# Performance work log

Measured on AMD Instinct MI355X. Metric: run time of the kernel, lower is better.

Reference implementation:

```python
import jax, jax.numpy as jnp
import numpy as np

B, DIM, N_SIDE = 32, 256, 32
HEADS, DIM_K, DIM_U = 4, 16, 1
DIM_V = 64  # dim_out // heads
EPS = 1e-5

def _rel_pos_idx(n):
    # matches calc_rel_pos: meshgrid(ij) -> (N,2), pairwise diff + (n-1)
    i = np.arange(n)
    pos = np.stack(np.meshgrid(i, i, indexing='ij'), 0).reshape(2, -1).T  # (N, 2)
    rel = pos[None, :] - pos[:, None] + (n - 1)                            # (N, N, 2)
    return rel[..., 0], rel[..., 1]

def _bn(t, gamma, beta):
    # BatchNorm2d in training mode: batch stats over (B, H, W), biased var
    mu = t.mean(axis=(0, 2, 3), keepdims=True)
    var = t.var(axis=(0, 2, 3), keepdims=True)
    xhat = (t - mu) * jax.lax.rsqrt(var + EPS)
    return xhat * gamma[None, :, None, None] + beta[None, :, None, None]

def setup_inputs() -> dict:
    key = jax.random.key(0)
    ks = jax.random.split(key, 5)
    rl = 2 * N_SIDE - 1
    return {
        'x': jax.random.normal(ks[0], (B, DIM, N_SIDE, N_SIDE), jnp.float32),
        'w_q': jax.random.normal(ks[1], (DIM_K * HEADS, DIM), jnp.float32) * 0.05,
        'w_k': jax.random.normal(ks[2], (DIM_K * DIM_U, DIM), jnp.float32) * 0.05,
        'w_v': jax.random.normal(ks[3], (DIM_V * DIM_U, DIM), jnp.float32) * 0.05,
        'gamma_q': jnp.ones((DIM_K * HEADS,), jnp.float32),
        'beta_q': jnp.zeros((DIM_K * HEADS,), jnp.float32),
        'gamma_v': jnp.ones((DIM_V * DIM_U,), jnp.float32),
        'beta_v': jnp.zeros((DIM_V * DIM_U,), jnp.float32),
        'rel_pos_emb': jax.random.normal(ks[4], (rl, rl, DIM_K, DIM_U), jnp.float32),
    }

def reference(x, w_q, w_k, w_v, gamma_q, beta_q, gamma_v, beta_v, rel_pos_emb):
    b, c, hh, ww = x.shape
    n = hh * ww
    # 1x1 convs as channel contractions
    q = _bn(jnp.einsum('oc,bchw->bohw', w_q, x), gamma_q, beta_q)
    k = jnp.einsum('oc,bchw->bohw', w_k, x)
    v = _bn(jnp.einsum('oc,bchw->bohw', w_v, x), gamma_v, beta_v)
    q = q.reshape(b, HEADS, DIM_K, n)   # b h k n
    k = k.reshape(b, DIM_U, DIM_K, n)   # b u k m
    v = v.reshape(b, DIM_U, DIM_V, n)   # b u v m
    k = jax.nn.softmax(k, axis=-1)
    # content lambda
    lam_c = jnp.einsum('bukm,buvm->bkv', k, v)
    Yc = jnp.einsum('bhkn,bkv->bhvn', q, lam_c)
    # positional lambda via relative-position embedding gather
    ni, mi = _rel_pos_idx(N_SIDE)
    emb = rel_pos_emb[ni, mi]                      # (n, n, k, u)
    lam_p = jnp.einsum('nmku,buvm->bnkv', emb, v)  # dominant compute
    Yp = jnp.einsum('bhkn,bnkv->bhvn', q, lam_p)
    Y = Yc + Yp                                    # b h v n
    return Y.reshape(b, HEADS * DIM_V, hh, ww)
```

## Files before the change

### kernel.cpp

```cpp
#include <hip/hip_runtime.h>

using u16 = unsigned short;
using u32 = unsigned int;

typedef __attribute__((ext_vector_type(4))) float f32x4;
typedef __attribute__((ext_vector_type(4))) u16 u16x4;
typedef __attribute__((ext_vector_type(8))) u16 u16x8;
typedef __attribute__((ext_vector_type(8))) short s16x8;

__device__ __forceinline__ u16 f2bf(float f) {
  u32 x = __builtin_bit_cast(u32, f);
  x += 0x7fffu + ((x >> 16) & 1u);
  return (u16)(x >> 16);
}
__device__ __forceinline__ float bf2f(u16 u) {
  u32 x = ((u32)u) << 16;
  return __builtin_bit_cast(float, x);
}

__device__ __forceinline__ void glds16(const u16* gsrc, u16* ldst) {
  __builtin_amdgcn_global_load_lds(
      (const __attribute__((address_space(1))) unsigned int*)gsrc,
      (__attribute__((address_space(3))) unsigned int*)ldst, 16, 0, 0);
}

__global__ __launch_bounds__(256) void k_prep(
    const float* __restrict__ wq, const float* __restrict__ wk,
    const float* __restrict__ wv, const float* __restrict__ R,
    u16* __restrict__ Wb, u16* __restrict__ APre)
{
  const int blk = blockIdx.x;
  const int t = threadIdx.x;
  if (blk < 144) {
    const int o = blk;
    const float* src = (o < 64) ? (wq + o * 256)
                     : (o < 80) ? (wk + (o - 64) * 256)
                                : (wv + (o - 80) * 256);
    Wb[o * 256 + t] = f2bf(src[t]);
  } else {
    const int di = blk - 144;
    const int w = t >> 6, l = t & 63;
    const int g = l >> 4, k = l & 15;
    for (int j1 = w; j1 < 32; j1 += 4) {
      u16x8 o8;
#pragma unroll
      for (int e = 0; e < 8; ++e) {
        int dj = 8 * g + e - j1 + 31;
        o8[e] = f2bf(R[(di * 63 + dj) * 16 + k]);
      }
      *(u16x8*)(APre + ((di * 32 + j1) * 64 + l) * 8) = o8;
    }
  }
}

union ProjSmem {
  u16 XLb[64][264];
  float SS[2][160];
};

__global__ __launch_bounds__(256) void k_proj(
    const float* __restrict__ x, const u16* __restrict__ Wb,
    float* __restrict__ q_raw, float* __restrict__ k_raw,
    float* __restrict__ v_raw,
    float* __restrict__ qs1, float* __restrict__ qs2,
    float* __restrict__ vs1, float* __restrict__ vs2)
{
  __shared__ ProjSmem PS;
  const int b  = blockIdx.x >> 4;
  const int p0 = (blockIdx.x & 15) * 64;
  const int t  = threadIdx.x;

  {
    const int p4 = (t & 15) * 4;
    const int cb = (t >> 4);
#pragma unroll
    for (int i = 0; i < 8; ++i) {
      const int c = 2 * (i * 16 + cb);
      f32x4 xa = *(const f32x4*)&x[(b * 256 + c) * 1024 + p0 + p4];
      f32x4 xb = *(const f32x4*)&x[(b * 256 + c + 1) * 1024 + p0 + p4];
#pragma unroll
      for (int j = 0; j < 4; ++j) {
        u32 pk = (u32)f2bf(xa[j]) | ((u32)f2bf(xb[j]) << 16);
        *(u32*)&PS.XLb[p4 + j][c] = pk;
      }
    }
  }
  __syncthreads();

  const int w  = t >> 6;
  const int l  = t & 63;
  const int g  = l >> 4;
  const int cc = l & 15;
  const int p  = p0 + w * 16 + cc;

  f32x4 acc[9];
  const f32x4 fz = {0.f, 0.f, 0.f, 0.f};
#pragma unroll
  for (int mt = 0; mt < 9; ++mt) acc[mt] = fz;

#pragma unroll
  for (int ko = 0; ko < 8; ++ko) {
    s16x8 bfr = *(const s16x8*)&PS.XLb[w * 16 + cc][ko * 32 + g * 8];
#pragma unroll
    for (int mt = 0; mt < 9; ++mt) {
      s16x8 afr = *(const s16x8*)&Wb[(mt * 16 + cc) * 256 + ko * 32 + g * 8];
      acc[mt] = __builtin_amdgcn_mfma_f32_16x16x32_bf16(afr, bfr, acc[mt], 0, 0, 0);
    }
  }

#pragma unroll
  for (int mt = 0; mt < 9; ++mt) {
#pragma unroll
    for (int r = 0; r < 4; ++r) {
      const int o = mt * 16 + 4 * g + r;
      const float val = acc[mt][r];
      if (mt < 4)       q_raw[(b * 64 + o) * 1024 + p] = val;
      else if (mt == 4) k_raw[(b * 16 + (o - 64)) * 1024 + p] = val;
      else              v_raw[(b * 64 + (o - 80)) * 1024 + p] = val;
    }
  }

  __syncthreads();
  {
    float* ss = &PS.SS[0][0];
    for (int i = t; i < 320; i += 256) ss[i] = 0.f;
  }
  __syncthreads();
#pragma unroll
  for (int mt = 0; mt < 9; ++mt) {
    if (mt == 4) continue;
#pragma unroll
    for (int r = 0; r < 4; ++r) {
      float s1 = acc[mt][r];
      float s2 = s1 * s1;
#pragma unroll
      for (int off = 1; off < 16; off <<= 1) {
        s1 += __shfl_xor(s1, off);
        s2 += __shfl_xor(s2, off);
      }
      if (cc == 0) {
        const int o = mt * 16 + 4 * g + r;
        atomicAdd(&PS.SS[0][o], s1);
        atomicAdd(&PS.SS[1][o], s2);
      }
    }
  }
  __syncthreads();
  if (t < 64) {
    atomicAdd(&qs1[t], PS.SS[0][t]);
    atomicAdd(&qs2[t], PS.SS[1][t]);
  } else if (t >= 80 && t < 144) {
    atomicAdd(&vs1[t - 80], PS.SS[0][t]);
    atomicAdd(&vs2[t - 80], PS.SS[1][t]);
  }
}

__global__ __launch_bounds__(256) void k_soft(
    const float* __restrict__ k_raw,
    float* __restrict__ kmax, float* __restrict__ kinv)
{
  const int t = threadIdx.x;
  const int w = t >> 6, lane = t & 63;
  const int row = blockIdx.x * 4 + w;
  const f32x4* kr4 = (const f32x4*)(k_raw + row * 1024 + lane * 16);
  f32x4 a0 = kr4[0], a1 = kr4[1], a2 = kr4[2], a3 = kr4[3];
  float mx = -3.0e38f;
#pragma unroll
  for (int j = 0; j < 4; ++j)
    mx = fmaxf(mx, fmaxf(fmaxf(a0[j], a1[j]), fmaxf(a2[j], a3[j])));
#pragma unroll
  for (int off = 32; off; off >>= 1) mx = fmaxf(mx, __shfl_xor(mx, off));
  float s = 0.f;
#pragma unroll
  for (int j = 0; j < 4; ++j)
    s += __expf(a0[j] - mx) + __expf(a1[j] - mx)
       + __expf(a2[j] - mx) + __expf(a3[j] - mx);
#pragma unroll
  for (int off = 32; off; off >>= 1) s += __shfl_xor(s, off);
  if (lane == 0) { kmax[row] = mx; kinv[row] = 1.0f / s; }
}

__global__ __launch_bounds__(256) void k_nl(
    const float* __restrict__ v_raw,
    const float* __restrict__ vs1, const float* __restrict__ vs2,
    const float* __restrict__ gv, const float* __restrict__ bv,
    const float* __restrict__ k_raw, const float* __restrict__ kmax,
    const float* __restrict__ kinv,
    u16* __restrict__ vnF, float* __restrict__ lam_c)
{
  __shared__ float VN[64][136];
  __shared__ float KE[16][132];
  const int b  = blockIdx.x >> 3;
  const int m0 = (blockIdx.x & 7) * 128;
  const int t  = threadIdx.x;
  {
    const int v = t & 63, mseg = t >> 6;
    const float invN = 1.0f / 32768.0f;
    const float mu = vs1[v] * invN;
    const float var = vs2[v] * invN - mu * mu;
    const float sc = rsqrtf(var + 1e-5f) * gv[v];
    const float bi = bv[v] - mu * sc;
    const int i2 = (m0 >> 5) + mseg;
    const float* src = v_raw + (b * 64 + v) * 1024 + i2 * 32;
    u16* dstF = vnF + ((b * 32 + i2) * 4 + (v >> 4)) * 512 + (v & 15) * 8;
#pragma unroll
    for (int lg = 0; lg < 4; ++lg) {
      f32x4 a = *(const f32x4*)(src + lg * 8);
      f32x4 c = *(const f32x4*)(src + lg * 8 + 4);
      f32x4 na, nc;
      u16x8 o8;
#pragma unroll
      for (int j = 0; j < 4; ++j) {
        na[j] = a[j] * sc + bi;
        nc[j] = c[j] * sc + bi;
        o8[j] = f2bf(na[j]);
        o8[4 + j] = f2bf(nc[j]);
      }
      *(f32x4*)&VN[v][mseg * 32 + lg * 8] = na;
      *(f32x4*)&VN[v][mseg * 32 + lg * 8 + 4] = nc;
      *(u16x8*)(dstF + lg * 128) = o8;
    }
  }
  {
    const int kc = t >> 4, mm = (t & 15) * 8;
    const int row = b * 16 + kc;
    const float* kr = k_raw + row * 1024 + m0 + mm;
    const float mx = kmax[row], iv = kinv[row];
#pragma unroll
    for (int j = 0; j < 8; ++j) KE[kc][mm + j] = __expf(kr[j] - mx) * iv;
  }
  __syncthreads();
  const int kc = t & 15, vg = t >> 4;
  float acc[4] = {0.f, 0.f, 0.f, 0.f};
  for (int m4 = 0; m4 < 128; m4 += 4) {
    f32x4 ke = *(const f32x4*)&KE[kc][m4];
#pragma unroll
    for (int j = 0; j < 4; ++j) {
      f32x4 vv = *(const f32x4*)&VN[vg * 4 + j][m4];
      acc[j] += ke[0] * vv[0] + ke[1] * vv[1] + ke[2] * vv[2] + ke[3] * vv[3];
    }
  }
#pragma unroll
  for (int j = 0; j < 4; ++j)
    atomicAdd(&lam_c[(b * 16 + kc) * 64 + vg * 4 + j], acc[j]);
}

__device__ __forceinline__ void load_a4(s16x8 (&dst)[4], const u16* ab)
{
#pragma unroll
  for (int j = 0; j < 4; ++j) dst[j] = *(const s16x8*)(ab + j * 512);
}

union KMainSmem {
  u16 BB[2][8192];
  float YL[256][18];
};

__global__ __launch_bounds__(256, 4) void k_main(
    const u16* __restrict__ APre, const u16* __restrict__ vnF,
    const float* __restrict__ q_raw, const float* __restrict__ lam_c,
    const float* __restrict__ qs1, const float* __restrict__ qs2,
    const float* __restrict__ gq, const float* __restrict__ bq,
    float* __restrict__ out)
{
  __shared__ alignas(16) KMainSmem S;
  __shared__ float QL[64][17];
  const int bid  = blockIdx.x;
  const int xcd  = bid & 7;
  const int sb   = bid >> 3;
  const int b    = xcd * 4 + (sb & 3);
  const int rest = sb >> 2;
  const int i1   = rest >> 1;
  const int half = rest & 1;
  const int t  = threadIdx.x;
  const int w  = t >> 6;
  const int l  = t & 63;
  const int g  = l >> 4;
  const int c  = l & 15;
  const int j1base = half * 16 + w * 4;

  const u16* vF = vnF + b * 65536;

  f32x4 acc[4][4];
  const f32x4 fz = {0.f, 0.f, 0.f, 0.f};
#pragma unroll
  for (int nn = 0; nn < 4; ++nn)
#pragma unroll
    for (int tt = 0; tt < 4; ++tt) acc[nn][tt] = fz;

  {
    const int o = t >> 2, ns = (t & 3) * 4;
    const float invN = 1.0f / 32768.0f;
    const float mu = qs1[o] * invN;
    const float var = qs2[o] * invN - mu * mu;
    const float rs = rsqrtf(var + 1e-5f);
    const float sc = rs * gq[o];
    const float bi = bq[o] - mu * sc;
    f32x4 qa = *(const f32x4*)&q_raw[(b * 64 + o) * 1024 + i1 * 32 + half * 16 + ns];
#pragma unroll
    for (int j = 0; j < 4; ++j) QL[o][ns + j] = qa[j] * sc + bi;
  }
  {
    const u16* src = vF + w * 2048 + l * 8;
    u16* dst = &S.BB[0][w * 2048];
#pragma unroll
    for (int j = 0; j < 4; ++j) glds16(src + j * 512, dst + j * 512);
  }

  s16x8 afrP[4], afrQ[4];
  const u16* aBase = APre + ((31 - i1) * 32 + j1base) * 512 + l * 8;
  load_a4(afrP, aBase);
  __syncthreads();

  for (int p = 0; p < 8; ++p) {
    const int cur = p & 1;
    const bool pf = (p < 7);
    if (pf) {
      const u16* src = vF + (p + 1) * 8192 + w * 2048 + l * 8;
      u16* dst = &S.BB[cur ^ 1][w * 2048];
#pragma unroll
      for (int j = 0; j < 4; ++j) glds16(src + j * 512, dst + j * 512);
    }
    __builtin_amdgcn_sched_barrier(0);
    const u16* ap = aBase + 4 * p * 16384;
    s16x8 bfr[4];
#pragma unroll
    for (int s = 0; s < 4; ++s) {
#pragma unroll
      for (int tt = 0; tt < 4; ++tt)
        bfr[tt] = *(const s16x8*)&S.BB[cur][s * 2048 + tt * 512 + l * 8];
      if (s < 3) {
        if (s & 1) load_a4(afrP, ap + (s + 1) * 16384);
        else       load_a4(afrQ, ap + (s + 1) * 16384);
      } else if (pf) {
        load_a4(afrP, ap + 4 * 16384);
      }
      const s16x8* A = (s & 1) ? afrQ : afrP;
#pragma unroll
      for (int nn = 0; nn < 4; ++nn)
#pragma unroll
        for (int tt = 0; tt < 4; ++tt)
          acc[nn][tt] = __builtin_amdgcn_mfma_f32_16x16x32_bf16(
              A[nn], bfr[tt], acc[nn][tt], 0, 0, 0);
    }
    asm volatile("s_waitcnt vmcnt(4)" ::: "memory");
    __builtin_amdgcn_sched_barrier(0);
    __builtin_amdgcn_s_barrier();
    __builtin_amdgcn_sched_barrier(0);
  }

  {
    const float* lcb = lam_c + b * 1024;
#pragma unroll
    for (int tt = 0; tt < 4; ++tt)
#pragma unroll
      for (int r = 0; r < 4; ++r) {
        const float lv = lcb[(4 * g + r) * 64 + tt * 16 + c];
#pragma unroll
        for (int nn = 0; nn < 4; ++nn) acc[nn][tt][r] += lv;
      }
  }
#pragma unroll
  for (int nn = 0; nn < 4; ++nn) {
    const int j1loc = w * 4 + nn;
#pragma unroll
    for (int h = 0; h < 4; ++h) {
      const float q0 = QL[h * 16 + 4 * g + 0][j1loc];
      const float q1 = QL[h * 16 + 4 * g + 1][j1loc];
      const float q2 = QL[h * 16 + 4 * g + 2][j1loc];
      const float q3 = QL[h * 16 + 4 * g + 3][j1loc];
#pragma unroll
      for (int tt = 0; tt < 4; ++tt) {
        float sY = q0 * acc[nn][tt][0] + q1 * acc[nn][tt][1]
                 + q2 * acc[nn][tt][2] + q3 * acc[nn][tt][3];
        sY += __shfl_xor(sY, 16);
        sY += __shfl_xor(sY, 32);
        if (g == h) S.YL[h * 64 + tt * 16 + c][j1loc] = sY;
      }
    }
  }
  __syncthreads();
#pragma unroll
  for (int it = 0; it < 4; ++it) {
    const int o  = (t >> 2) + it * 64;
    const int nf = (t & 3) * 4;
    f32x4 v4 = *(const f32x4*)&S.YL[o][nf];
    *(f32x4*)&out[(b * 256 + o) * 1024 + i1 * 32 + half * 16 + nf] = v4;
  }
}

extern "C" void kernel_launch(void* const* d_in, const int* in_sizes, int n_in,
                              void* d_out, int out_size, void* d_ws, size_t ws_size,
                              hipStream_t stream) {
  const float* x  = (const float*)d_in[0];
  const float* wq = (const float*)d_in[1];
  const float* wk = (const float*)d_in[2];
  const float* wv = (const float*)d_in[3];
  const float* gq = (const float*)d_in[4];
  const float* bq = (const float*)d_in[5];
  const float* gv = (const float*)d_in[6];
  const float* bv = (const float*)d_in[7];
  const float* R  = (const float*)d_in[8];
  float* out = (float*)d_out;

  float* wsf   = (float*)d_ws;
  float* q_raw = wsf;
  float* k_raw = q_raw + 32 * 64 * 1024;
  float* v_raw = k_raw + 32 * 16 * 1024;
  float* lam_c = v_raw + 32 * 64 * 1024;
  float* qs1   = lam_c + 32 * 16 * 64;
  float* qs2   = qs1 + 64;
  float* vs1   = qs2 + 64;
  float* vs2   = vs1 + 64;
  float* kmax  = vs2 + 64;
  float* kinv  = kmax + 512;
  u16*   vn    = (u16*)(kinv + 512);
  u16*   vnF   = vn + 32 * 64 * 1024;
  u16*   APre  = vnF + 32 * 65536;
  u16*   Wb    = APre + 63 * 32 * 512;

  hipMemsetAsync(lam_c, 0, (32 * 16 * 64 + 256) * sizeof(float), stream);
  k_prep<<<207, 256, 0, stream>>>(wq, wk, wv, R, Wb, APre);
  k_proj<<<512, 256, 0, stream>>>(x, Wb, q_raw, k_raw, v_raw, qs1, qs2, vs1, vs2);
  k_soft<<<128, 256, 0, stream>>>(k_raw, kmax, kinv);
  k_nl<<<256, 256, 0, stream>>>(v_raw, vs1, vs2, gv, bv, k_raw, kmax, kinv, vnF, lam_c);
  k_main<<<2048, 256, 0, stream>>>(APre, vnF, q_raw, lam_c, qs1, qs2, gq, bq, out);
}
```

Baseline: 138.3 us.

## Process two batches per k_main block to reuse positional-embedding A fragments

```diff
diff --git a/kernel.cpp b/kernel.cpp
--- a/kernel.cpp
+++ b/kernel.cpp
@@ -252,11 +252,11 @@
 }
 
 union KMainSmem {
-  u16 BB[2][8192];
+  u16 BB[2][16384];
   float YL[256][18];
 };
 
-__global__ __launch_bounds__(256, 4) void k_main(
+__global__ __launch_bounds__(256, 2) void k_main(
     const u16* __restrict__ APre, const u16* __restrict__ vnF,
     const float* __restrict__ q_raw, const float* __restrict__ lam_c,
     const float* __restrict__ qs1, const float* __restrict__ qs2,
@@ -264,14 +264,15 @@
     float* __restrict__ out)
 {
   __shared__ alignas(16) KMainSmem S;
-  __shared__ float QL[64][17];
+  __shared__ float QL[2][64][17];
   const int bid  = blockIdx.x;
   const int xcd  = bid & 7;
   const int sb   = bid >> 3;
-  const int b    = xcd * 4 + (sb & 3);
-  const int rest = sb >> 2;
+  const int pl   = sb & 1;
+  const int rest = sb >> 1;
   const int i1   = rest >> 1;
   const int half = rest & 1;
+  const int b0   = xcd * 4 + pl * 2;
   const int t  = threadIdx.x;
   const int w  = t >> 6;
   const int l  = t & 63;
@@ -279,113 +280,124 @@
   const int c  = l & 15;
   const int j1base = half * 16 + w * 4;
 
-  const u16* vF = vnF + b * 65536;
-
-  f32x4 acc[4][4];
+  f32x4 acc[2][4][4];
   const f32x4 fz = {0.f, 0.f, 0.f, 0.f};
 #pragma unroll
-  for (int nn = 0; nn < 4; ++nn)
-#pragma unroll
-    for (int tt = 0; tt < 4; ++tt) acc[nn][tt] = fz;
-
+  for (int bb = 0; bb < 2; ++bb)
+#pragma unroll
+    for (int nn = 0; nn < 4; ++nn)
+#pragma unroll
+      for (int tt = 0; tt < 4; ++tt) acc[bb][nn][tt] = fz;
+
+  const int i2s_w = w >> 1, bsel_w = w & 1;
+  auto stage = [&](int ph, int buf) {
+    const u16* src = vnF + (b0 + bsel_w) * 65536 + (2 * ph + i2s_w) * 2048 + l * 8;
+    u16* dst = &S.BB[buf][(i2s_w * 2 + bsel_w) * 2048];
+#pragma unroll
+    for (int j = 0; j < 4; ++j) glds16(src + j * 512, dst + j * 512);
+  };
+
+  stage(0, 0);
   {
     const int o = t >> 2, ns = (t & 3) * 4;
     const float invN = 1.0f / 32768.0f;
     const float mu = qs1[o] * invN;
     const float var = qs2[o] * invN - mu * mu;
-    const float rs = rsqrtf(var + 1e-5f);
-    const float sc = rs * gq[o];
+    const float sc = rsqrtf(var + 1e-5f) * gq[o];
     const float bi = bq[o] - mu * sc;
-    f32x4 qa = *(const f32x4*)&q_raw[(b * 64 + o) * 1024 + i1 * 32 + half * 16 + ns];
-#pragma unroll
-    for (int j = 0; j < 4; ++j) QL[o][ns + j] = qa[j] * sc + bi;
-  }
-  {
-    const u16* src = vF + w * 2048 + l * 8;
-    u16* dst = &S.BB[0][w * 2048];
-#pragma unroll
-    for (int j = 0; j < 4; ++j) glds16(src + j * 512, dst + j * 512);
-  }
-
+#pragma unroll
+    for (int bb = 0; bb < 2; ++bb) {
+      f32x4 qa = *(const f32x4*)&q_raw[((b0 + bb) * 64 + o) * 1024
+                                       + i1 * 32 + half * 16 + ns];
+#pragma unroll
+      for (int j = 0; j < 4; ++j) QL[bb][o][ns + j] = qa[j] * sc + bi;
+    }
+  }
   s16x8 afrP[4], afrQ[4];
-  const u16* aBase = APre + ((31 - i1) * 32 + j1base) * 512 + l * 8;
-  load_a4(afrP, aBase);
-  __syncthreads();
-
-  for (int p = 0; p < 8; ++p) {
+  const u16* aB = APre + ((31 - i1) * 32 + j1base) * 512 + l * 8;
+  load_a4(afrP, aB);
+  __syncthreads();
+
+#define MFMA16(AF, BB_ACC)                                                    \
+  _Pragma("unroll")                                                           \
+  for (int nn = 0; nn < 4; ++nn)                                              \
+    _Pragma("unroll")                                                         \
+    for (int tt = 0; tt < 4; ++tt)                                            \
+      BB_ACC[nn][tt] = __builtin_amdgcn_mfma_f32_16x16x32_bf16(               \
+          AF[nn], bfr[tt], BB_ACC[nn][tt], 0, 0, 0);
+
+  for (int p = 0; p < 16; ++p) {
     const int cur = p & 1;
-    const bool pf = (p < 7);
-    if (pf) {
-      const u16* src = vF + (p + 1) * 8192 + w * 2048 + l * 8;
-      u16* dst = &S.BB[cur ^ 1][w * 2048];
-#pragma unroll
-      for (int j = 0; j < 4; ++j) glds16(src + j * 512, dst + j * 512);
-    }
+    const bool pf = (p < 15);
+    if (pf) stage(p + 1, cur ^ 1);
     __builtin_amdgcn_sched_barrier(0);
-    const u16* ap = aBase + 4 * p * 16384;
     s16x8 bfr[4];
-#pragma unroll
-    for (int s = 0; s < 4; ++s) {
-#pragma unroll
-      for (int tt = 0; tt < 4; ++tt)
-        bfr[tt] = *(const s16x8*)&S.BB[cur][s * 2048 + tt * 512 + l * 8];
-      if (s < 3) {
-        if (s & 1) load_a4(afrP, ap + (s + 1) * 16384);
-        else       load_a4(afrQ, ap + (s + 1) * 16384);
-      } else if (pf) {
-        load_a4(afrP, ap + 4 * 16384);
-      }
-      const s16x8* A = (s & 1) ? afrQ : afrP;
-#pragma unroll
-      for (int nn = 0; nn < 4; ++nn)
-#pragma unroll
-        for (int tt = 0; tt < 4; ++tt)
-          acc[nn][tt] = __builtin_amdgcn_mfma_f32_16x16x32_bf16(
-              A[nn], bfr[tt], acc[nn][tt], 0, 0, 0);
-    }
+    load_a4(afrQ, aB + (2 * p + 1) * 16384);
+#pragma unroll
+    for (int tt = 0; tt < 4; ++tt)
+      bfr[tt] = *(const s16x8*)&S.BB[cur][0 * 2048 + tt * 512 + l * 8];
+    MFMA16(afrP, acc[0])
+#pragma unroll
+    for (int tt = 0; tt < 4; ++tt)
+      bfr[tt] = *(const s16x8*)&S.BB[cur][1 * 2048 + tt * 512 + l * 8];
+    MFMA16(afrP, acc[1])
+    if (pf) load_a4(afrP, aB + (2 * p + 2) * 16384);
+#pragma unroll
+    for (int tt = 0; tt < 4; ++tt)
+      bfr[tt] = *(const s16x8*)&S.BB[cur][2 * 2048 + tt * 512 + l * 8];
+    MFMA16(afrQ, acc[0])
+#pragma unroll
+    for (int tt = 0; tt < 4; ++tt)
+      bfr[tt] = *(const s16x8*)&S.BB[cur][3 * 2048 + tt * 512 + l * 8];
+    MFMA16(afrQ, acc[1])
     asm volatile("s_waitcnt vmcnt(4)" ::: "memory");
     __builtin_amdgcn_sched_barrier(0);
     __builtin_amdgcn_s_barrier();
     __builtin_amdgcn_sched_barrier(0);
   }
-
-  {
-    const float* lcb = lam_c + b * 1024;
-#pragma unroll
-    for (int tt = 0; tt < 4; ++tt)
-#pragma unroll
-      for (int r = 0; r < 4; ++r) {
-        const float lv = lcb[(4 * g + r) * 64 + tt * 16 + c];
-#pragma unroll
-        for (int nn = 0; nn < 4; ++nn) acc[nn][tt][r] += lv;
-      }
-  }
-#pragma unroll
-  for (int nn = 0; nn < 4; ++nn) {
-    const int j1loc = w * 4 + nn;
-#pragma unroll
-    for (int h = 0; h < 4; ++h) {
-      const float q0 = QL[h * 16 + 4 * g + 0][j1loc];
-      const float q1 = QL[h * 16 + 4 * g + 1][j1loc];
-      const float q2 = QL[h * 16 + 4 * g + 2][j1loc];
-      const float q3 = QL[h * 16 + 4 * g + 3][j1loc];
-#pragma unroll
-      for (int tt = 0; tt < 4; ++tt) {
-        float sY = q0 * acc[nn][tt][0] + q1 * acc[nn][tt][1]
-                 + q2 * acc[nn][tt][2] + q3 * acc[nn][tt][3];
-        sY += __shfl_xor(sY, 16);
-        sY += __shfl_xor(sY, 32);
-        if (g == h) S.YL[h * 64 + tt * 16 + c][j1loc] = sY;
-      }
-    }
-  }
-  __syncthreads();
-#pragma unroll
-  for (int it = 0; it < 4; ++it) {
-    const int o  = (t >> 2) + it * 64;
-    const int nf = (t & 3) * 4;
-    f32x4 v4 = *(const f32x4*)&S.YL[o][nf];
-    *(f32x4*)&out[(b * 256 + o) * 1024 + i1 * 32 + half * 16 + nf] = v4;
+#undef MFMA16
+
+#pragma unroll
+  for (int bb = 0; bb < 2; ++bb) {
+    if (bb) __syncthreads();
+    {
+      const float* lcb = lam_c + (b0 + bb) * 1024;
+#pragma unroll
+      for (int tt = 0; tt < 4; ++tt)
+#pragma unroll
+        for (int r = 0; r < 4; ++r) {
+          const float lv = lcb[(4 * g + r) * 64 + tt * 16 + c];
+#pragma unroll
+          for (int nn = 0; nn < 4; ++nn) acc[bb][nn][tt][r] += lv;
+        }
+    }
+#pragma unroll
+    for (int nn = 0; nn < 4; ++nn) {
+      const int j1loc = w * 4 + nn;
+#pragma unroll
+      for (int h = 0; h < 4; ++h) {
+        const float q0 = QL[bb][h * 16 + 4 * g + 0][j1loc];
+        const float q1 = QL[bb][h * 16 + 4 * g + 1][j1loc];
+        const float q2 = QL[bb][h * 16 + 4 * g + 2][j1loc];
+        const float q3 = QL[bb][h * 16 + 4 * g + 3][j1loc];
+#pragma unroll
+        for (int tt = 0; tt < 4; ++tt) {
+          float sY = q0 * acc[bb][nn][tt][0] + q1 * acc[bb][nn][tt][1]
+                   + q2 * acc[bb][nn][tt][2] + q3 * acc[bb][nn][tt][3];
+          sY += __shfl_xor(sY, 16);
+          sY += __shfl_xor(sY, 32);
+          if (g == h) S.YL[h * 64 + tt * 16 + c][j1loc] = sY;
+        }
+      }
+    }
+    __syncthreads();
+#pragma unroll
+    for (int it = 0; it < 4; ++it) {
+      const int o  = (t >> 2) + it * 64;
+      const int nf = (t & 3) * 4;
+      f32x4 v4 = *(const f32x4*)&S.YL[o][nf];
+      *(f32x4*)&out[((b0 + bb) * 256 + o) * 1024 + i1 * 32 + half * 16 + nf] = v4;
+    }
   }
 }
 
@@ -424,5 +436,5 @@
   k_proj<<<512, 256, 0, stream>>>(x, Wb, q_raw, k_raw, v_raw, qs1, qs2, vs1, vs2);
   k_soft<<<128, 256, 0, stream>>>(k_raw, kmax, kinv);
   k_nl<<<256, 256, 0, stream>>>(v_raw, vs1, vs2, gv, bv, k_raw, kmax, kinv, vnF, lam_c);
-  k_main<<<2048, 256, 0, stream>>>(APre, vnF, q_raw, lam_c, qs1, qs2, gq, bq, out);
-}
+  k_main<<<1024, 256, 0, stream>>>(APre, vnF, q_raw, lam_c, qs1, qs2, gq, bq, out);
+}
```

Result: slower. 145.8 us (+5.5%).
